# Optimization experiments

Measured on AMD Instinct MI355X. Metric: run time of the kernel, lower is better.

## Reference

```python
import jax, jax.numpy as jnp
import numpy as np
from jax import lax

NUM_ROUTES = 3
OUT_CAPS = 8
OUT_CH = 16


def squash(t):
    # squared_norm * t / ((1 + squared_norm) * sqrt(squared_norm)), norm over last dim
    sn = jnp.sum(t * t, axis=-1, keepdims=True)
    return sn * t / ((1.0 + sn) * jnp.sqrt(sn))


def setup_inputs() -> dict:
    key = jax.random.key(0)
    k1, k2 = jax.random.split(key)
    x = jax.random.normal(k1, (16, 8, 16, 128, 128), dtype=jnp.float32)
    # conv weight [out_channels*out_capsules, in_channels, 4, 4], kaiming-ish scale
    W_conv = jax.random.normal(k2, (OUT_CH * OUT_CAPS, 16, 4, 4), dtype=jnp.float32) * 0.05
    b_conv = jnp.zeros((OUT_CH * OUT_CAPS,), dtype=jnp.float32)
    return {"x": x, "W_conv": W_conv, "b_conv": b_conv}


def reference(x, W_conv, b_conv):
    B, IC, Cin, W, H = x.shape
    xr = x.reshape(B * IC, Cin, W, H)
    u = lax.conv_general_dilated(
        xr, W_conv,
        window_strides=(2, 2), padding=((2, 2), (2, 2)),
        dimension_numbers=("NCHW", "OIHW", "NCHW"),
    ) + b_conv[None, :, None, None]
    ow, oh = u.shape[2], u.shape[3]
    # [B*IC, OC*Cout, ow, oh] -> [B, IC, ow, oh, OC, Cout]
    u_hat = u.transpose(0, 2, 3, 1).reshape(B, IC, ow, oh, OUT_CAPS, OUT_CH)

    b_ij = jnp.zeros((1, IC, ow, oh, OUT_CAPS), dtype=u_hat.dtype)
    v_j = None
    for it in range(NUM_ROUTES):
        c_ij = jax.nn.softmax(b_ij, axis=1)[..., None]      # [1,IC,ow,oh,OC,1]
        s_j = jnp.sum(c_ij * u_hat, axis=1)                  # [B,ow,oh,OC,Cout]
        v_j = squash(s_j)
        if it < NUM_ROUTES - 1:
            # agreement: dot over Cout between u_hat and v_j
            a_ij = jnp.einsum('biwhoc,bwhoc->biwho', u_hat, v_j)
            b_ij = b_ij + jnp.mean(a_ij, axis=0, keepdims=True)
    # [B,ow,oh,OC,Cout] -> [B, OC, Cout, ow, oh]
    return v_j.transpose(0, 3, 4, 1, 2)
```

## Files before the change

### kernel.cpp

```cpp
#include <hip/hip_runtime.h>
#include <math.h>

#define BB   16
#define IC   8
#define BI   128
#define CIN  16
#define WH   128
#define OWH  65
#define NPIX (OWH*OWH)
#define OC   8
#define COUT 16
#define NOC  128
#define KTOT 256
#define KC   64
#define NCHUNK 4
#define S_TOTAL (CIN*WH*WH)

#define NCHM 8

typedef unsigned short ushortT;
typedef __bf16 bf16x8 __attribute__((ext_vector_type(8)));
typedef float  f32x4  __attribute__((ext_vector_type(4)));

__device__ __forceinline__ ushortT f2bf(float f) {
    unsigned u = __float_as_uint(f);
    unsigned r = (u + 0x7fffu + ((u >> 16) & 1u)) >> 16;
    return (ushortT)r;
}

__global__ void cvtT_kernel(const float* __restrict__ x,
                            ushortT* __restrict__ xbfT)
{
    __shared__ ushortT tile[64 * 136];
    const int t  = threadIdx.x;
    const int s0 = blockIdx.x * 64;

#pragma unroll
    for (int k = 0; k < 8; ++k) {
        const int j  = t + k * 256;
        const int bi = j >> 4, s4 = j & 15;
        const float4 v = *(const float4*)(x + (size_t)bi * S_TOTAL + s0 + s4 * 4);
        const int si = s4 * 4;
        tile[(si    ) * 136 + (bi ^ (((si    ) & 15) << 3))] = f2bf(v.x);
        tile[(si + 1) * 136 + (bi ^ (((si + 1) & 15) << 3))] = f2bf(v.y);
        tile[(si + 2) * 136 + (bi ^ (((si + 2) & 15) << 3))] = f2bf(v.z);
        tile[(si + 3) * 136 + (bi ^ (((si + 3) & 15) << 3))] = f2bf(v.w);
    }
    __syncthreads();
#pragma unroll
    for (int k = 0; k < 4; ++k) {
        const int j  = t + k * 256;
        const int sI = j >> 4, g = j & 15;
        const uint4 val = *(const uint4*)&tile[sI * 136 + ((g ^ (sI & 15)) << 3)];
        *(uint4*)(xbfT + (size_t)(s0 + sI) * 128 + g * 8) = val;
    }
}

__global__ void prep_w_kernel(const float* __restrict__ W,
                              ushortT* __restrict__ Wbf)
{
    int idx = blockIdx.x * 256 + threadIdx.x;
    int oc = idx >> 8, k = idx & 255;
    int kpg = k >> 3, j = k & 7;
    Wbf[((size_t)kpg * 128 + oc) * 8 + j] = f2bf(W[idx]);
}

__launch_bounds__(512, 4)
__global__ void capsconv_mfma(const ushortT* __restrict__ xbfT,
                              const ushortT* __restrict__ Wbf,
                              const float* __restrict__ bias,
                              float* __restrict__ outbuf,
                              const int direct_out)
{
    __shared__ __align__(16) ushortT As[2][4 * 128 * 8];
    __shared__ __align__(16) ushortT Bs[2][4 * 128 * 8];
    __shared__ float cijs[64];
    __shared__ float bijs[64];
    __shared__ float aTmp[16 * 64];

    const int t  = threadIdx.x;
    const int g8 = blockIdx.x;
    int p = (g8 & 7) * 529 + (g8 >> 3);
    if (p >= NPIX) return;

    const int w  = t >> 6;
    const int ln = t & 63;
    const int q  = ln >> 4;
    const int cL = ln & 15;
    const int h  = q & 1;
    const int mrow_base = 64 * (w >> 2);
    const int ncol_base = 32 * (w & 3);

    const int px = p / OWH;
    const int py = p % OWH;
    const int row0 = 2 * px - 2;
    const int col0 = 2 * py - 2;

    f32x4 acc[4][2];
#pragma unroll
    for (int mt = 0; mt < 4; ++mt)
#pragma unroll
        for (int nt = 0; nt < 2; ++nt) acc[mt][nt] = (f32x4){0.f, 0.f, 0.f, 0.f};

    const int g     = t & 15;
    const int sI    = t >> 4;
    const int colw  = sI & 3;
    const int rowl  = (sI >> 2) & 3;
    const int cih   = sI >> 4;
    const int srow  = row0 + rowl;
    const int scol  = col0 + colw;
    const bool ok   = (srow >= 0 && srow < WH && scol >= 0 && scol < WH);
    const size_t aoff0 = ok
        ? ((size_t)((cih * WH + srow) * WH + scol) * 128 + g * 8)
        : 0;
    const int kpg   = cih * 2 + (rowl >> 1);
    const int jj    = (rowl & 1) * 4 + colw;
    const int wbase = (kpg * 128 + g * 8) * 16 + jj * 2;
    const int gk7   = g & 7;

    int aRd[4];
#pragma unroll
    for (int mt = 0; mt < 4; ++mt) {
        const int by = (q * 128 + mrow_base + mt * 16 + cL) * 16;
        aRd[mt] = by ^ (((by >> 7) & 7) << 4);
    }

    uint4 aR;
    uint4 bR;

    auto loadA = [&](int kc) {
        aR = make_uint4(0u, 0u, 0u, 0u);
        if (ok) aR = *(const uint4*)(xbfT + aoff0 + (size_t)kc * (2 * WH * WH * 128));
    };
    auto loadB = [&](int kc) {
        bR = ((const uint4*)Wbf)[kc * 512 + t];
    };
    auto storeAB = [&](int buf) {
        char* ab = (char*)&As[buf][0];
        const ushortT* av = (const ushortT*)&aR;
#pragma unroll
        for (int c = 0; c < 8; ++c)
            *(ushortT*)(ab + wbase + ((c ^ gk7) << 4)) = av[c];
        ((uint4*)Bs[buf])[t] = bR;
    };

    loadA(0); loadB(0);
    storeAB(0);

    for (int kc = 0; kc < NCHM; ++kc) {
        __syncthreads();
        if (kc < NCHM - 1) { loadA(kc + 1); loadB(kc + 1); }

        {
            const int buf = kc & 1;
            const char* abase = (const char*)&As[buf][0];
            bf16x8 af[4], bfr[2];
#pragma unroll
            for (int mt = 0; mt < 4; ++mt)
                af[mt] = *(const bf16x8*)(abase + aRd[mt]);
#pragma unroll
            for (int nt = 0; nt < 2; ++nt)
                bfr[nt] = *(const bf16x8*)&Bs[buf][(q * 128 + ncol_base + nt * 16 + cL) * 8];
#pragma unroll
            for (int mt = 0; mt < 4; ++mt)
#pragma unroll
                for (int nt = 0; nt < 2; ++nt)
                    acc[mt][nt] = __builtin_amdgcn_mfma_f32_16x16x32_bf16(
                        af[mt], bfr[nt], acc[mt][nt], 0, 0, 0);
        }

        if (kc < NCHM - 1) storeAB((kc + 1) & 1);
    }

#pragma unroll
    for (int nt = 0; nt < 2; ++nt) {
        const float bv = bias[ncol_base + nt * 16 + cL];
#pragma unroll
        for (int mt = 0; mt < 4; ++mt) acc[mt][nt] += bv;
    }

    for (int it = 0; it < 3; ++it) {
        float4 cf4[2];
        if (it == 0) {
#pragma unroll
            for (int nt = 0; nt < 2; ++nt)
                cf4[nt] = make_float4(0.125f, 0.125f, 0.125f, 0.125f);
        } else {
#pragma unroll
            for (int nt = 0; nt < 2; ++nt)
                cf4[nt] = *(const float4*)&cijs[(2 * (w & 3) + nt) * 8 + 4 * h];
        }

#pragma unroll
        for (int mt = 0; mt < 4; ++mt) {
            const int b = 8 * (w >> 2) + 2 * mt + (q >> 1);
#pragma unroll
            for (int nt = 0; nt < 2; ++nt) {
                const int o = 2 * (w & 3) + nt;
                const float4 cf = cf4[nt];
                float sp = cf.x * acc[mt][nt][0] + cf.y * acc[mt][nt][1]
                         + cf.z * acc[mt][nt][2] + cf.w * acc[mt][nt][3];
                float s = sp + __shfl_xor(sp, 16);
                float ssq = s * s;
#pragma unroll
                for (int d = 1; d < 16; d <<= 1) ssq += __shfl_xor(ssq, d);
                const float scale = sqrtf(ssq) * __builtin_amdgcn_rcpf(1.f + ssq);
                const float vj = s * scale;

                if (it == 2) {
                    if (q == 0 || q == 2) {
                        if (direct_out)
                            outbuf[(size_t)(b * NOC + o * 16 + cL) * NPIX + p] = vj;
                        else
                            outbuf[(size_t)p * 2048 + b * NOC + o * 16 + cL] = vj;
                    }
                } else {
                    f32x4 ap = acc[mt][nt] * vj;
#pragma unroll
                    for (int d = 1; d < 16; d <<= 1) {
                        ap[0] += __shfl_xor(ap[0], d);
                        ap[1] += __shfl_xor(ap[1], d);
                        ap[2] += __shfl_xor(ap[2], d);
                        ap[3] += __shfl_xor(ap[3], d);
                    }
                    if (cL == 0) {
                        float* dst = &aTmp[b * 64 + o * 8 + 4 * h];
                        dst[0] = ap[0]; dst[1] = ap[1]; dst[2] = ap[2]; dst[3] = ap[3];
                    }
                }
            }
        }
        if (it < 2) {
            __syncthreads();
            if (t < 64) {
                float sum = 0.f;
#pragma unroll
                for (int b = 0; b < BB; ++b) sum += aTmp[b * 64 + t];
                float bij = (it == 0 ? 0.f : bijs[t]) + sum * (1.f / 16.f);
                bijs[t] = bij;
                float mx = bij;
                mx = fmaxf(mx, __shfl_xor(mx, 1));
                mx = fmaxf(mx, __shfl_xor(mx, 2));
                mx = fmaxf(mx, __shfl_xor(mx, 4));
                float e = __expf(bij - mx);
                float se = e;
                se += __shfl_xor(se, 1);
                se += __shfl_xor(se, 2);
                se += __shfl_xor(se, 4);
                cijs[t] = e * __builtin_amdgcn_rcpf(se);
            }
            __syncthreads();
        }
    }
}

__global__ void transpose_kernel(const float* __restrict__ vtmp,
                                 float* __restrict__ out)
{
    __shared__ float tile[32][33];
    const int bp = blockIdx.x;
    const int bc = blockIdx.y;
    const int p0 = bp * 32, c0 = bc * 32;
    const int tx = threadIdx.x & 31, ty = threadIdx.x >> 5;

    for (int r = ty; r < 32; r += 8) {
        const int p = p0 + r;
        tile[r][tx] = (p < NPIX) ? vtmp[(size_t)p * 2048 + c0 + tx] : 0.f;
    }
    __syncthreads();
    for (int r = ty; r < 32; r += 8) {
        const int c = c0 + r;
        const int p = p0 + tx;
        if (p < NPIX) out[(size_t)c * NPIX + p] = tile[tx][r];
    }
}

__launch_bounds__(256, 2)
__global__ void capsconv_fp32(const float* __restrict__ x,
                              const float* __restrict__ Wc,
                              const float* __restrict__ bias,
                              float* __restrict__ outbuf,
                              const int direct_out)
{
    __shared__ float As[KC][BI];
    __shared__ float Bsh[KC][NOC];
    __shared__ float cij[64];
    __shared__ float bijs2[64];
    __shared__ float aTmp2[BB * 64];

    const int t  = threadIdx.x;
    const int tn = t & 15;
    const int tm = t >> 4;
    const int p  = blockIdx.x;
    const int px = p / OWH;
    const int py = p % OWH;
    const int row0 = 2 * px - 2;
    const int col0 = 2 * py - 2;
    const bool interior = (px >= 1 && px <= 63 && py >= 1 && py <= 63);

    float C[8][8];
#pragma unroll
    for (int r = 0; r < 8; ++r)
#pragma unroll
        for (int j = 0; j < 8; ++j) C[r][j] = 0.f;

    float areg[8][4];
    float breg[32];

    auto load_chunk = [&](int kc) {
#pragma unroll
        for (int g = 0; g < 8; ++g) {
            const int L    = g * 256 + t;
            const int bi   = L & 127;
            const int cikw = L >> 7;
            const int ci   = kc * 4 + (cikw >> 2);
            const int kw   = cikw & 3;
            const int row  = row0 + kw;
            const float* src = x + (((size_t)(bi * CIN + ci) * WH + row) * WH + col0);
            if (interior) {
                const float2 v01 = *(const float2*)(src);
                const float2 v23 = *(const float2*)(src + 2);
                areg[g][0] = v01.x; areg[g][1] = v01.y;
                areg[g][2] = v23.x; areg[g][3] = v23.y;
            } else {
#pragma unroll
                for (int kh = 0; kh < 4; ++kh) {
                    const int col = col0 + kh;
                    areg[g][kh] = (row >= 0 && row < WH && col >= 0 && col < WH)
                                      ? src[kh] : 0.f;
                }
            }
        }
        {
            const int oc  = t >> 1;
            const int kk0 = (t & 1) * 32;
            const float* wsrc = Wc + (size_t)oc * KTOT + kc * KC + kk0;
#pragma unroll
            for (int m = 0; m < 32; m += 4) {
                const float4 v = *(const float4*)(wsrc + m);
                breg[m] = v.x; breg[m+1] = v.y; breg[m+2] = v.z; breg[m+3] = v.w;
            }
        }
    };

    load_chunk(0);
    for (int kc = 0; kc < NCHUNK; ++kc) {
        __syncthreads();
#pragma unroll
        for (int g = 0; g < 8; ++g) {
            const int L    = g * 256 + t;
            const int bi   = L & 127;
            const int cikw = L >> 7;
            const int kkb  = cikw * 4;
#pragma unroll
            for (int kh = 0; kh < 4; ++kh) As[kkb + kh][bi] = areg[g][kh];
        }
        {
            const int oc  = t >> 1;
            const int kk0 = (t & 1) * 32;
#pragma unroll
            for (int m = 0; m < 32; ++m) Bsh[kk0 + m][oc] = breg[m];
        }
        __syncthreads();
        if (kc < NCHUNK - 1) load_chunk(kc + 1);
#pragma unroll 4
        for (int k = 0; k < KC; ++k) {
            float af[8], bf[8];
            *(float4*)(af)     = *(const float4*)&As[k][tm * 8];
            *(float4*)(af + 4) = *(const float4*)&As[k][tm * 8 + 4];
            *(float4*)(bf)     = *(const float4*)&Bsh[k][tn * 8];
            *(float4*)(bf + 4) = *(const float4*)&Bsh[k][tn * 8 + 4];
#pragma unroll
            for (int r = 0; r < 8; ++r)
#pragma unroll
                for (int j = 0; j < 8; ++j)
                    C[r][j] = fmaf(af[r], bf[j], C[r][j]);
        }
    }
#pragma unroll
    for (int j = 0; j < 8; ++j) {
        const float bj = bias[tn * 8 + j];
#pragma unroll
        for (int r = 0; r < 8; ++r) C[r][j] += bj;
    }

    const int o = tn >> 1;
    __syncthreads();
    if (t < 64) bijs2[t] = 0.f;

    float vout[8];
    for (int it = 0; it < 3; ++it) {
        __syncthreads();
        if (t < 8) {
            const int oo = t;
            float mx = -1e30f;
#pragma unroll
            for (int i = 0; i < 8; ++i) mx = fmaxf(mx, bijs2[i * 8 + oo]);
            float e[8]; float ssum = 0.f;
#pragma unroll
            for (int i = 0; i < 8; ++i) { e[i] = expf(bijs2[i * 8 + oo] - mx); ssum += e[i]; }
            const float inv = 1.f / ssum;
#pragma unroll
            for (int i = 0; i < 8; ++i) cij[i * 8 + oo] = e[i] * inv;
        }
        __syncthreads();
        float cf[8];
#pragma unroll
        for (int i = 0; i < 8; ++i) cf[i] = cij[i * 8 + o];
        float s[8];
#pragma unroll
        for (int j = 0; j < 8; ++j) {
            float acc = 0.f;
#pragma unroll
            for (int r = 0; r < 8; ++r) acc = fmaf(cf[r], C[r][j], acc);
            s[j] = acc;
        }
        float ssq = 0.f;
#pragma unroll
        for (int j = 0; j < 8; ++j) ssq = fmaf(s[j], s[j], ssq);
        ssq += __shfl_xor(ssq, 1);
        const float scale = ssq / ((1.f + ssq) * sqrtf(ssq));
        if (it == 2) {
#pragma unroll
            for (int j = 0; j < 8; ++j) vout[j] = s[j] * scale;
        } else {
            float ap[8];
#pragma unroll
            for (int r = 0; r < 8; ++r) {
                float acc = 0.f;
#pragma unroll
                for (int j = 0; j < 8; ++j) acc = fmaf(C[r][j], s[j] * scale, acc);
                ap[r] = acc;
            }
#pragma unroll
            for (int r = 0; r < 8; ++r) ap[r] += __shfl_xor(ap[r], 1);
            if ((tn & 1) == 0) {
#pragma unroll
                for (int r = 0; r < 8; ++r) aTmp2[tm * 64 + r * 8 + o] = ap[r];
            }
            __syncthreads();
            if (t < 64) {
                float acc = 0.f;
#pragma unroll
                for (int b = 0; b < BB; ++b) acc += aTmp2[b * 64 + t];
                bijs2[t] += acc * (1.f / 16.f);
            }
        }
    }
    if (direct_out) {
#pragma unroll
        for (int j = 0; j < 8; ++j)
            outbuf[(size_t)(tm * NOC + tn * 8 + j) * NPIX + p] = vout[j];
    } else {
        float4* dst = (float4*)(outbuf + (size_t)p * 2048 + tm * NOC + tn * 8);
        dst[0] = make_float4(vout[0], vout[1], vout[2], vout[3]);
        dst[1] = make_float4(vout[4], vout[5], vout[6], vout[7]);
    }
}

extern "C" void kernel_launch(void* const* d_in, const int* in_sizes, int n_in,
                              void* d_out, int out_size, void* d_ws, size_t ws_size,
                              hipStream_t stream)
{
    const float* x    = (const float*)d_in[0];
    const float* Wc   = (const float*)d_in[1];
    const float* bias = (const float*)d_in[2];
    float* out        = (float*)d_out;

    const size_t VT_BYTES = (size_t)NPIX * 2048 * sizeof(float);
    const size_t WB_OFF   = VT_BYTES;
    const size_t XB_OFF   = WB_OFF + 65536;
    const size_t TOTAL    = XB_OFF + (size_t)BI * CIN * WH * WH * 2;

    if (ws_size >= TOTAL) {
        ushortT* Wbf  = (ushortT*)((char*)d_ws + WB_OFF);
        ushortT* xbfT = (ushortT*)((char*)d_ws + XB_OFF);

        cvtT_kernel<<<S_TOTAL / 64, 256, 0, stream>>>(x, xbfT);
        prep_w_kernel<<<128, 256, 0, stream>>>(Wc, Wbf);
        capsconv_mfma<<<529 * 8, 512, 0, stream>>>(xbfT, Wbf, bias, out, 1);
    } else if (ws_size >= VT_BYTES) {
        float* vtmp = (float*)d_ws;
        capsconv_fp32<<<NPIX, 256, 0, stream>>>(x, Wc, bias, vtmp, 0);
        dim3 g((NPIX + 31) / 32, 2048 / 32);
        transpose_kernel<<<g, 256, 0, stream>>>(vtmp, out);
    } else {
        capsconv_fp32<<<NPIX, 256, 0, stream>>>(x, Wc, bias, out, 1);
    }
}
```

Before: 418.9 us.

## Read conv weights directly from global and triple-buffer input tiles in LDS

```diff
diff --git a/kernel.cpp b/kernel.cpp
--- a/kernel.cpp
+++ b/kernel.cpp
@@ -72,8 +72,7 @@
                               float* __restrict__ outbuf,
                               const int direct_out)
 {
-    __shared__ __align__(16) ushortT As[2][4 * 128 * 8];
-    __shared__ __align__(16) ushortT Bs[2][4 * 128 * 8];
+    __shared__ __align__(16) ushortT As[3][4 * 128 * 8];
     __shared__ float cijs[64];
     __shared__ float bijs[64];
     __shared__ float aTmp[16 * 64];
@@ -125,42 +124,38 @@
         aRd[mt] = by ^ (((by >> 7) & 7) << 4);
     }
 
-    uint4 aR;
-    uint4 bR;
-
-    auto loadA = [&](int kc) {
-        aR = make_uint4(0u, 0u, 0u, 0u);
-        if (ok) aR = *(const uint4*)(xbfT + aoff0 + (size_t)kc * (2 * WH * WH * 128));
+    uint4 aR[2];
+
+    auto loadA = [&](uint4& r, int kc) {
+        r = make_uint4(0u, 0u, 0u, 0u);
+        if (ok) r = *(const uint4*)(xbfT + aoff0 + (size_t)kc * (2 * WH * WH * 128));
     };
-    auto loadB = [&](int kc) {
-        bR = ((const uint4*)Wbf)[kc * 512 + t];
-    };
-    auto storeAB = [&](int buf) {
+    auto storeA = [&](int buf, const uint4& r) {
         char* ab = (char*)&As[buf][0];
-        const ushortT* av = (const ushortT*)&aR;
+        const ushortT* av = (const ushortT*)&r;
 #pragma unroll
         for (int c = 0; c < 8; ++c)
             *(ushortT*)(ab + wbase + ((c ^ gk7) << 4)) = av[c];
-        ((uint4*)Bs[buf])[t] = bR;
     };
 
-    loadA(0); loadB(0);
-    storeAB(0);
-
+    loadA(aR[0], 0);
+    loadA(aR[1], 1);
+    storeA(0, aR[0]);
+    loadA(aR[0], 2);
+    __syncthreads();
+
+#pragma unroll
     for (int kc = 0; kc < NCHM; ++kc) {
-        __syncthreads();
-        if (kc < NCHM - 1) { loadA(kc + 1); loadB(kc + 1); }
-
+        const int buf = kc % 3;
         {
-            const int buf = kc & 1;
             const char* abase = (const char*)&As[buf][0];
             bf16x8 af[4], bfr[2];
 #pragma unroll
             for (int mt = 0; mt < 4; ++mt)
                 af[mt] = *(const bf16x8*)(abase + aRd[mt]);
-#pragma unroll
-            for (int nt = 0; nt < 2; ++nt)
-                bfr[nt] = *(const bf16x8*)&Bs[buf][(q * 128 + ncol_base + nt * 16 + cL) * 8];
+            const ushortT* bsrc = Wbf + kc * 4096 + (q * 128 + ncol_base + cL) * 8;
+            bfr[0] = *(const bf16x8*)(bsrc);
+            bfr[1] = *(const bf16x8*)(bsrc + 128);
 #pragma unroll
             for (int mt = 0; mt < 4; ++mt)
 #pragma unroll
@@ -168,8 +163,9 @@
                     acc[mt][nt] = __builtin_amdgcn_mfma_f32_16x16x32_bf16(
                         af[mt], bfr[nt], acc[mt][nt], 0, 0, 0);
         }
-
-        if (kc < NCHM - 1) storeAB((kc + 1) & 1);
+        if (kc + 1 < NCHM) storeA((kc + 1) % 3, aR[(kc + 1) & 1]);
+        if (kc + 3 < NCHM) loadA(aR[(kc + 3) & 1], kc + 3);
+        __syncthreads();
     }
 
 #pragma unroll
```

Result: no change. 411.5 us (-1.8%).
